# Performance work log

Hardware: AMD Instinct MI355X
Metric: run time of the kernel (lower is better)

## Reference

```python
import jax, jax.numpy as jnp
import numpy as np

EMB = 1024
FFN = 4096
H = 16
HD = EMB // H
EPS = 1e-6
SLOPE = 0.01


def leaky_relu(x):
    return jnp.where(x >= 0, x, SLOPE * x)


def layer_norm(x, g, b):
    mu = jnp.mean(x, axis=-1, keepdims=True)
    var = jnp.mean((x - mu) ** 2, axis=-1, keepdims=True)
    return (x - mu) * jax.lax.rsqrt(var + EPS) * g + b


def setup_inputs() -> dict:
    key = jax.random.key(0)
    ks = jax.random.split(key, 16)
    B, N = 2, 2048
    x = jax.random.normal(ks[0], (B, N, EMB), dtype=jnp.float32)

    def lin(k, fan_in, fan_out, kaiming_normal):
        kw, kb = jax.random.split(k)
        gain = float(np.sqrt(2.0 / (1.0 + SLOPE ** 2)))
        if kaiming_normal:
            W = jax.random.normal(kw, (fan_out, fan_in)) * (gain / np.sqrt(fan_in))
        else:
            bound = gain * np.sqrt(3.0 / fan_in)
            W = jax.random.uniform(kw, (fan_out, fan_in), minval=-bound, maxval=bound)
        b = jax.random.normal(kb, (fan_out,)) * 1e-6
        return W.astype(jnp.float32), b.astype(jnp.float32)

    Wq, bq = lin(ks[1], EMB, EMB, True)
    Wk, bk = lin(ks[2], EMB, EMB, True)
    Wv, bv = lin(ks[3], EMB, EMB, True)
    Wo, bo = lin(ks[4], EMB, EMB, True)
    W1, b1 = lin(ks[5], EMB, FFN, False)
    W2, b2 = lin(ks[6], FFN, EMB, False)
    return {
        "x": x,
        "ln1_g": jnp.ones((EMB,)), "ln1_b": jnp.zeros((EMB,)),
        "ln2_g": jnp.ones((EMB,)), "ln2_b": jnp.zeros((EMB,)),
        "Wq": Wq, "bq": bq, "Wk": Wk, "bk": bk, "Wv": Wv, "bv": bv,
        "Wo": Wo, "bo": bo, "W1": W1, "b1": b1, "W2": W2, "b2": b2,
    }


def reference(x, ln1_g, ln1_b, ln2_g, ln2_b, Wq, bq, Wk, bk, Wv, bv, Wo, bo, W1, b1, W2, b2):
    B, N, _ = x.shape
    h = x
    xn = layer_norm(x, ln1_g, ln1_b)
    # QKV projections, split heads: [B, H, N, HD]
    def heads(t):
        return t.reshape(B, N, H, HD).transpose(0, 2, 1, 3)
    q = heads(xn @ Wq.T + bq)
    k = heads(xn @ Wk.T + bk)
    v = heads(xn @ Wv.T + bv)
    scores = jnp.einsum('bhnd,bhmd->bhnm', q, k) / jnp.sqrt(jnp.float32(HD))
    probs = leaky_relu(scores)  # non-softmax attention
    ctx = jnp.einsum('bhnm,bhmd->bhnd', probs, v)
    ctx = ctx.transpose(0, 2, 1, 3).reshape(B, N, EMB)
    attn_out = ctx @ Wo.T + bo
    x = attn_out + h
    h = x
    xn = layer_norm(x, ln2_g, ln2_b)
    ff = leaky_relu(xn @ W1.T + b1) @ W2.T + b2
    return ff + h
```

## Files before the change

### kernel.cpp

```cpp
#include <hip/hip_runtime.h>
#include <hip/hip_bf16.h>


typedef unsigned short u16;
typedef __bf16 bf16x8 __attribute__((ext_vector_type(8)));
typedef float f32x4 __attribute__((ext_vector_type(4)));
typedef unsigned short u16x8 __attribute__((ext_vector_type(8)));

typedef const __attribute__((address_space(1))) void* as1cv;
typedef __attribute__((address_space(3))) void* as3v;

#define MFMA16(a, b, c) __builtin_amdgcn_mfma_f32_16x16x32_bf16((a), (b), (c), 0, 0, 0)
#define GLL16(g, l) __builtin_amdgcn_global_load_lds((as1cv)(g), (as3v)(l), 16, 0, 0)

__device__ __forceinline__ u16 f2bf(float f) {
  unsigned u = __builtin_bit_cast(unsigned, f);
  u += 0x7fffu + ((u >> 16) & 1u);
  return (u16)(u >> 16);
}
__device__ __forceinline__ float bf2f(u16 u) {
  return __builtin_bit_cast(float, ((unsigned)u) << 16);
}
__device__ __forceinline__ float lrelu(float v) { return v >= 0.f ? v : 0.01f * v; }

__device__ __forceinline__ int xcds(int bid, int nwg) {
  int cpx = nwg >> 3;
  return (bid & 7) * cpx + (bid >> 3);
}

__global__ __launch_bounds__(256) void cvt6(
    const float* __restrict__ p0, const float* __restrict__ p1,
    const float* __restrict__ p2, const float* __restrict__ p3,
    const float* __restrict__ p4, const float* __restrict__ p5,
    u16* __restrict__ o0, u16* __restrict__ o1, u16* __restrict__ o2,
    u16* __restrict__ o3, u16* __restrict__ o4, u16* __restrict__ o5)
{
  int i = blockIdx.x * 256 + threadIdx.x;
  const float* src; u16* dst; int off;
  if (i < 4 * 131072) {
    int s = i >> 17; off = i & 131071;
    src = (s == 0) ? p0 : (s == 1) ? p1 : (s == 2) ? p2 : p3;
    dst = (s == 0) ? o0 : (s == 1) ? o1 : (s == 2) ? o2 : o3;
  } else {
    int j = i - 4 * 131072;
    int s = j >> 19; off = j & 524287;
    src = s ? p5 : p4;
    dst = s ? o5 : o4;
  }
  const float4* s4 = (const float4*)src;
  float4 a = s4[(size_t)off * 2], b = s4[(size_t)off * 2 + 1];
  u16x8 o = { f2bf(a.x), f2bf(a.y), f2bf(a.z), f2bf(a.w),
              f2bf(b.x), f2bf(b.y), f2bf(b.z), f2bf(b.w) };
  *(u16x8*)(dst + (size_t)off * 8) = o;
}

__global__ __launch_bounds__(256) void ln_k(
    const float* __restrict__ x, const float* __restrict__ g,
    const float* __restrict__ bb, u16* __restrict__ out)
{
  const int tid = threadIdx.x;
  const int row = blockIdx.x;
  const float4* xr = (const float4*)(x + (size_t)row * 1024);
  float4 v = xr[tid];
  float s  = v.x + v.y + v.z + v.w;
  float s2 = v.x*v.x + v.y*v.y + v.z*v.z + v.w*v.w;
#pragma unroll
  for (int o = 32; o > 0; o >>= 1) { s += __shfl_down(s, o, 64); s2 += __shfl_down(s2, o, 64); }
  __shared__ float sh[8];
  if ((tid & 63) == 0) { sh[tid >> 6] = s; sh[4 + (tid >> 6)] = s2; }
  __syncthreads();
  s  = sh[0] + sh[1] + sh[2] + sh[3];
  s2 = sh[4] + sh[5] + sh[6] + sh[7];
  float mu  = s * (1.0f / 1024.0f);
  float var = s2 * (1.0f / 1024.0f) - mu * mu;
  float rs  = rsqrtf(var + 1e-6f);
  float4 gv = ((const float4*)g)[tid];
  float4 bv = ((const float4*)bb)[tid];
  ushort4 o;
  o.x = f2bf((v.x - mu) * rs * gv.x + bv.x);
  o.y = f2bf((v.y - mu) * rs * gv.y + bv.y);
  o.z = f2bf((v.z - mu) * rs * gv.z + bv.z);
  o.w = f2bf((v.w - mu) * rs * gv.w + bv.w);
  ((ushort4*)out)[(size_t)row * 256 + tid] = o;
}

__device__ __forceinline__ void gemm_core128(
    const u16* __restrict__ A, const u16* __restrict__ W,
    int kstride, int klen,
    int row0, int wrow0, u16* lsA, u16* lsB, f32x4 (&acc)[4][4])
{
  const int tid  = threadIdx.x;
  const int lane = tid & 63, wave = tid >> 6;
  const int wr = wave >> 1, wc = wave & 1;
  const int lr = lane & 15, lg = lane >> 4;

  const u16* ga0 = A + (size_t)(row0 + (tid >> 2)) * kstride + (tid & 3) * 8;
  const u16* ga1 = ga0 + (size_t)64 * kstride;
  const u16* gb0 = W + (size_t)(wrow0 + (tid >> 2)) * kstride + (tid & 3) * 8;
  const u16* gb1 = gb0 + (size_t)64 * kstride;
  u16* la = lsA + tid * 8;
  u16* lb = lsB + tid * 8;

  GLL16(ga0, la); GLL16(ga1, la + 2048);
  GLL16(gb0, lb); GLL16(gb1, lb + 2048);
  ga0 += 32; ga1 += 32; gb0 += 32; gb1 += 32;
  __syncthreads();

  const int nsteps = klen >> 5;
  int cur = 0;
  for (int t = 0; t < nsteps; t++) {
    int nxt = cur ^ 1;
    if (t + 1 < nsteps) {
      GLL16(ga0, la + nxt * 4096);
      GLL16(ga1, la + nxt * 4096 + 2048);
      GLL16(gb0, lb + nxt * 4096);
      GLL16(gb1, lb + nxt * 4096 + 2048);
      ga0 += 32; ga1 += 32; gb0 += 32; gb1 += 32;
    }
    const u16* cA = lsA + cur * 4096;
    const u16* cB = lsB + cur * 4096;
    bf16x8 av[4], bv[4];
#pragma unroll
    for (int mi = 0; mi < 4; mi++)
      av[mi] = *reinterpret_cast<const bf16x8*>(cA + (wr * 64 + mi * 16 + lr) * 32 + lg * 8);
#pragma unroll
    for (int ni = 0; ni < 4; ni++)
      bv[ni] = *reinterpret_cast<const bf16x8*>(cB + (wc * 64 + ni * 16 + lr) * 32 + lg * 8);
#pragma unroll
    for (int mi = 0; mi < 4; mi++)
#pragma unroll
      for (int ni = 0; ni < 4; ni++)
        acc[mi][ni] = MFMA16(av[mi], bv[ni], acc[mi][ni]);
    __syncthreads();
    cur = nxt;
  }
}

__global__ __launch_bounds__(256, 4) void gemm_qkv(
    const u16* __restrict__ xn,
    const u16* __restrict__ Wq, const u16* __restrict__ Wk, const u16* __restrict__ Wv,
    const float* __restrict__ bq, const float* __restrict__ bk, const float* __restrict__ bv,
    u16* __restrict__ qb, u16* __restrict__ kb, u16* __restrict__ vtb)
{
  __shared__ u16 lsA[2 * 128 * 32];
  __shared__ u16 lsB[2 * 128 * 32];
  const int wid = xcds(blockIdx.x, 768);
  const int mt = wid / 24, nt = wid % 24;
  const int row0 = mt * 128, col0 = nt * 128;
  const int sel = col0 >> 10, c0 = col0 & 1023;
  const u16* W = (sel == 0) ? Wq : (sel == 1) ? Wk : Wv;
  const float* bias = (sel == 0) ? bq : (sel == 1) ? bk : bv;

  f32x4 acc[4][4];
  f32x4 z = {0.f, 0.f, 0.f, 0.f};
#pragma unroll
  for (int mi = 0; mi < 4; mi++)
#pragma unroll
    for (int ni = 0; ni < 4; ni++) acc[mi][ni] = z;

  gemm_core128(xn, W, 1024, 1024, row0, c0, lsA, lsB, acc);

  const int lane = threadIdx.x & 63, wave = threadIdx.x >> 6;
  const int wr = wave >> 1, wc = wave & 1;
  const int lr = lane & 15, lg = lane >> 4;
#pragma unroll
  for (int ni = 0; ni < 4; ni++) {
    int c = c0 + wc * 64 + ni * 16 + lr;
    float bsv = bias[c];
    int h = c >> 6, hd = c & 63;
#pragma unroll
    for (int mi = 0; mi < 4; mi++) {
      int rbase = row0 + wr * 64 + mi * 16 + lg * 4;
      int b = rbase >> 11;
      int n = rbase & 2047;
      if (sel < 2) {
        u16* dst = (sel == 0) ? qb : kb;
        size_t base = ((size_t)(b * 16 + h) * 2048 + n) * 64 + hd;
#pragma unroll
        for (int r = 0; r < 4; r++)
          dst[base + (size_t)r * 64] = f2bf(acc[mi][ni][r] + bsv);
      } else {
        size_t base = ((size_t)((b * 16 + h) * 64 + hd)) * 2048 + n;
        ushort4 o;
        o.x = f2bf(acc[mi][ni][0] + bsv);
        o.y = f2bf(acc[mi][ni][1] + bsv);
        o.z = f2bf(acc[mi][ni][2] + bsv);
        o.w = f2bf(acc[mi][ni][3] + bsv);
        *(ushort4*)(vtb + base) = o;
      }
    }
  }
}

template <int EPI>
__global__ __launch_bounds__(256, 4) void gemm128(
    const u16* __restrict__ A, const u16* __restrict__ W,
    const float* __restrict__ bias, float* __restrict__ outf,
    u16* __restrict__ outh, const float* __restrict__ extra,
    int K, int nTiles, int nwg)
{
  __shared__ u16 lsA[2 * 128 * 32];
  __shared__ u16 lsB[2 * 128 * 32];
  const int wid = xcds(blockIdx.x, nwg);
  const int mt = wid / nTiles, nt = wid % nTiles;
  const int row0 = mt * 128, col0 = nt * 128;

  f32x4 acc[4][4];
  f32x4 z = {0.f, 0.f, 0.f, 0.f};
#pragma unroll
  for (int mi = 0; mi < 4; mi++)
#pragma unroll
    for (int ni = 0; ni < 4; ni++) acc[mi][ni] = z;

  gemm_core128(A, W, K, K, row0, col0, lsA, lsB, acc);

  const int N = nTiles * 128;
  const int lane = threadIdx.x & 63, wave = threadIdx.x >> 6;
  const int wr = wave >> 1, wc = wave & 1;
  const int lr = lane & 15, lg = lane >> 4;
#pragma unroll
  for (int ni = 0; ni < 4; ni++) {
    int col = col0 + wc * 64 + ni * 16 + lr;
    float bsv = bias[col];
#pragma unroll
    for (int mi = 0; mi < 4; mi++) {
      int rbase = row0 + wr * 64 + mi * 16 + lg * 4;
#pragma unroll
      for (int r = 0; r < 4; r++) {
        float v = acc[mi][ni][r] + bsv;
        size_t idx = (size_t)(rbase + r) * N + col;
        if (EPI == 0) {
          outf[idx] = v + extra[idx];
        } else {
          outh[idx] = f2bf(lrelu(v));
        }
      }
    }
  }
}

__global__ __launch_bounds__(256, 4) void gemm_ffn2(
    const u16* __restrict__ A, const u16* __restrict__ W,
    u16* __restrict__ pout)
{
  __shared__ u16 lsA[2 * 128 * 32];
  __shared__ u16 lsB[2 * 128 * 32];
  const int wid = xcds(blockIdx.x, 1024);
  const int chunk = wid >> 8, rem = wid & 255;
  const int mt = rem >> 3, nt = rem & 7;
  const int row0 = mt * 128, col0 = nt * 128;

  f32x4 acc[4][4];
  f32x4 z = {0.f, 0.f, 0.f, 0.f};
#pragma unroll
  for (int mi = 0; mi < 4; mi++)
#pragma unroll
    for (int ni = 0; ni < 4; ni++) acc[mi][ni] = z;

  gemm_core128(A + chunk * 1024, W + chunk * 1024, 4096, 1024,
               row0, col0, lsA, lsB, acc);

  u16* out = pout + (size_t)chunk * (4096 * 1024);
  const int lane = threadIdx.x & 63, wave = threadIdx.x >> 6;
  const int wr = wave >> 1, wc = wave & 1;
  const int lr = lane & 15, lg = lane >> 4;
#pragma unroll
  for (int ni = 0; ni < 4; ni++) {
    int col = col0 + wc * 64 + ni * 16 + lr;
#pragma unroll
    for (int mi = 0; mi < 4; mi++) {
      int rbase = row0 + wr * 64 + mi * 16 + lg * 4;
#pragma unroll
      for (int r = 0; r < 4; r++)
        out[(size_t)(rbase + r) * 1024 + col] = f2bf(acc[mi][ni][r]);
    }
  }
}

__global__ __launch_bounds__(256) void reduce_ffn2(
    const u16* __restrict__ p, const float* __restrict__ b2,
    const float* __restrict__ x2, float* __restrict__ out)
{
  size_t i = ((size_t)blockIdx.x * 256 + threadIdx.x) * 4;
  int col = (int)(i & 1023);
  ushort4 a0 = *(const ushort4*)(p + i);
  ushort4 a1 = *(const ushort4*)(p + (size_t)(4096 * 1024) + i);
  ushort4 a2 = *(const ushort4*)(p + (size_t)(2 * 4096 * 1024) + i);
  ushort4 a3 = *(const ushort4*)(p + (size_t)(3 * 4096 * 1024) + i);
  float4 bv = *(const float4*)(b2 + col);
  float4 xv = *(const float4*)(x2 + i);
  float4 r;
  r.x = bf2f(a0.x) + bf2f(a1.x) + bf2f(a2.x) + bf2f(a3.x) + bv.x + xv.x;
  r.y = bf2f(a0.y) + bf2f(a1.y) + bf2f(a2.y) + bf2f(a3.y) + bv.y + xv.y;
  r.z = bf2f(a0.z) + bf2f(a1.z) + bf2f(a2.z) + bf2f(a3.z) + bv.z + xv.z;
  r.w = bf2f(a0.w) + bf2f(a1.w) + bf2f(a2.w) + bf2f(a3.w) + bv.w + xv.w;
  *(float4*)(out + i) = r;
}

__device__ __forceinline__ int swz(int row, int col) {
  return row * 64 + (col ^ ((row & 7) << 3));
}

__global__ __launch_bounds__(256, 3) void attn_k(
    const u16* __restrict__ qb, const u16* __restrict__ kb,
    const u16* __restrict__ vtb, u16* __restrict__ ctx)
{
  __shared__ u16 lq[128 * 64];
  __shared__ u16 lk[64 * 64];
  __shared__ u16 lv[64 * 64];
  __shared__ u16 lp[128 * 64];

  const int tid = threadIdx.x;
  const int lane = tid & 63, wave = tid >> 6;
  const int wr = wave >> 1, wc = wave & 1;
  const int lr = lane & 15, lg = lane >> 4;
  const int wid = xcds(blockIdx.x, 512);
  const int bh = wid >> 4, qt = wid & 15;
  const int n0 = qt * 128;
  const u16* qh = qb + (size_t)bh * 2048 * 64;
  const u16* kh = kb + (size_t)bh * 2048 * 64;
  const u16* vh = vtb + (size_t)bh * 64 * 2048;

  {
    int r = tid >> 3, kk = (tid & 7) * 8;
#pragma unroll
    for (int j = 0; j < 4; j++)
      *(u16x8*)(lq + swz(j * 32 + r, kk)) =
          *(const u16x8*)(qh + (size_t)(n0 + j * 32 + r) * 64 + kk);
  }

  f32x4 z = {0.f, 0.f, 0.f, 0.f};
  f32x4 cacc[4][2];
#pragma unroll
  for (int mi = 0; mi < 4; mi++)
#pragma unroll
    for (int ni = 0; ni < 2; ni++) cacc[mi][ni] = z;

  for (int kt = 0; kt < 32; kt++) {
    {
      int r = tid >> 3, kk = (tid & 7) * 8;
#pragma unroll
      for (int j = 0; j < 2; j++) {
        *(u16x8*)(lk + swz(j * 32 + r, kk)) =
            *(const u16x8*)(kh + (size_t)(kt * 64 + j * 32 + r) * 64 + kk);
        *(u16x8*)(lv + swz(j * 32 + r, kk)) =
            *(const u16x8*)(vh + (size_t)(j * 32 + r) * 2048 + kt * 64 + kk);
      }
    }
    __syncthreads();

    f32x4 sacc[4][2];
#pragma unroll
    for (int mi = 0; mi < 4; mi++)
#pragma unroll
      for (int ni = 0; ni < 2; ni++) sacc[mi][ni] = z;
#pragma unroll
    for (int ks = 0; ks < 2; ks++) {
      bf16x8 aq[4], bk8[2];
#pragma unroll
      for (int mi = 0; mi < 4; mi++)
        aq[mi] = *reinterpret_cast<const bf16x8*>(lq + swz(wr * 64 + mi * 16 + lr, ks * 32 + lg * 8));
#pragma unroll
      for (int ni = 0; ni < 2; ni++)
        bk8[ni] = *reinterpret_cast<const bf16x8*>(lk + swz(wc * 32 + ni * 16 + lr, ks * 32 + lg * 8));
#pragma unroll
      for (int mi = 0; mi < 4; mi++)
#pragma unroll
        for (int ni = 0; ni < 2; ni++)
          sacc[mi][ni] = MFMA16(aq[mi], bk8[ni], sacc[mi][ni]);
    }
#pragma unroll
    for (int mi = 0; mi < 4; mi++)
#pragma unroll
      for (int ni = 0; ni < 2; ni++)
#pragma unroll
        for (int r = 0; r < 4; r++) {
          float v = lrelu(sacc[mi][ni][r] * 0.125f);
          int i = wr * 64 + mi * 16 + lg * 4 + r;
          int j = wc * 32 + ni * 16 + lr;
          lp[swz(i, j)] = f2bf(v);
        }
    __syncthreads();

#pragma unroll
    for (int js = 0; js < 2; js++) {
      bf16x8 pa[4], vb[2];
#pragma unroll
      for (int mi = 0; mi < 4; mi++)
        pa[mi] = *reinterpret_cast<const bf16x8*>(lp + swz(wr * 64 + mi * 16 + lr, js * 32 + lg * 8));
#pragma unroll
      for (int ni = 0; ni < 2; ni++)
        vb[ni] = *reinterpret_cast<const bf16x8*>(lv + swz(wc * 32 + ni * 16 + lr, js * 32 + lg * 8));
#pragma unroll
      for (int mi = 0; mi < 4; mi++)
#pragma unroll
        for (int ni = 0; ni < 2; ni++)
          cacc[mi][ni] = MFMA16(pa[mi], vb[ni], cacc[mi][ni]);
    }
    __syncthreads();
  }

  const int b = bh >> 4, h = bh & 15;
#pragma unroll
  for (int mi = 0; mi < 4; mi++)
#pragma unroll
    for (int ni = 0; ni < 2; ni++)
#pragma unroll
      for (int r = 0; r < 4; r++) {
        int n = n0 + wr * 64 + mi * 16 + lg * 4 + r;
        int d = wc * 32 + ni * 16 + lr;
        ctx[((size_t)(b * 2048 + n)) * 1024 + h * 64 + d] = f2bf(cacc[mi][ni][r]);
      }
}

extern "C" void kernel_launch(void* const* d_in, const int* in_sizes, int n_in,
                              void* d_out, int out_size, void* d_ws, size_t ws_size,
                              hipStream_t stream) {
  (void)in_sizes; (void)n_in; (void)out_size; (void)ws_size;
  const float* x    = (const float*)d_in[0];
  const float* ln1g = (const float*)d_in[1];
  const float* ln1b = (const float*)d_in[2];
  const float* ln2g = (const float*)d_in[3];
  const float* ln2b = (const float*)d_in[4];
  const float* Wq = (const float*)d_in[5];  const float* bq = (const float*)d_in[6];
  const float* Wk = (const float*)d_in[7];  const float* bk = (const float*)d_in[8];
  const float* Wv = (const float*)d_in[9];  const float* bv = (const float*)d_in[10];
  const float* Wo = (const float*)d_in[11]; const float* bo = (const float*)d_in[12];
  const float* W1 = (const float*)d_in[13]; const float* b1 = (const float*)d_in[14];
  const float* W2 = (const float*)d_in[15]; const float* b2 = (const float*)d_in[16];

  char* ws = (char*)d_ws;
  u16*   WqB  = (u16*)(ws + ((size_t)0 << 20));
  u16*   WkB  = (u16*)(ws + ((size_t)2 << 20));
  u16*   WvB  = (u16*)(ws + ((size_t)4 << 20));
  u16*   WoB  = (u16*)(ws + ((size_t)6 << 20));
  u16*   W1B  = (u16*)(ws + ((size_t)8 << 20));
  u16*   W2B  = (u16*)(ws + ((size_t)16 << 20));
  u16*   xn1  = (u16*)(ws + ((size_t)24 << 20));
  u16*   qb   = (u16*)(ws + ((size_t)32 << 20));
  u16*   kb   = (u16*)(ws + ((size_t)40 << 20));
  u16*   vtb  = (u16*)(ws + ((size_t)48 << 20));
  u16*   ctxb = (u16*)(ws + ((size_t)56 << 20));
  float* x2   = (float*)(ws + ((size_t)64 << 20));
  u16*   xn2  = (u16*)(ws + ((size_t)80 << 20));
  u16*   ff1  = (u16*)(ws + ((size_t)88 << 20));
  u16*   pF2  = (u16*)(ws + ((size_t)24 << 20));

  dim3 blk(256);

  cvt6<<<dim3(6144), blk, 0, stream>>>(Wq, Wk, Wv, Wo, W1, W2,
                                       WqB, WkB, WvB, WoB, W1B, W2B);
  ln_k<<<dim3(4096), blk, 0, stream>>>(x, ln1g, ln1b, xn1);
  gemm_qkv<<<dim3(768), blk, 0, stream>>>(xn1, WqB, WkB, WvB, bq, bk, bv,
                                          qb, kb, vtb);
  attn_k<<<dim3(512), blk, 0, stream>>>(qb, kb, vtb, ctxb);
  gemm128<0><<<dim3(256), blk, 0, stream>>>(ctxb, WoB, bo, x2, (u16*)nullptr, x,
                                            1024, 8, 256);
  ln_k<<<dim3(4096), blk, 0, stream>>>(x2, ln2g, ln2b, xn2);
  gemm128<1><<<dim3(1024), blk, 0, stream>>>(xn2, W1B, b1, (float*)nullptr, ff1,
                                             (const float*)nullptr, 1024, 32, 1024);
  gemm_ffn2<<<dim3(1024), blk, 0, stream>>>(ff1, W2B, pF2);
  reduce_ffn2<<<dim3(4096), blk, 0, stream>>>(pF2, b2, x2, (float*)d_out);
}
```

Measured before the change: 353.4 us.

## Rewrite attention kernel with register-resident Q, transposed scores, and async KV pipeline

The attention kernel now keeps each wave's Q rows in registers and computes transposed score tiles (K·Q). Their MFMA output layout feeds straight into a 16x16x16 MFMA against V^T as the B operand, so the LDS round-trip for the probability matrix goes away. K/V tiles are streamed with global_load_lds into a 4-deep ring buffer with manual vmcnt waits and a single barrier per tile, replacing three __syncthreads per tile. The 1/sqrt(d) scale is folded into the Q projection epilogue and leaky ReLU becomes fmax. The cost is more LDS per block, occupancy lowered to 2 blocks, and more MFMA instructions from the smaller-K variant.

```diff
diff --git a/kernel.cpp b/kernel.cpp
--- a/kernel.cpp
+++ b/kernel.cpp
@@ -3,9 +3,13 @@
 
 
 typedef unsigned short u16;
+typedef unsigned int u32;
 typedef __bf16 bf16x8 __attribute__((ext_vector_type(8)));
+typedef __bf16 bf16x4 __attribute__((ext_vector_type(4)));
 typedef float f32x4 __attribute__((ext_vector_type(4)));
 typedef unsigned short u16x8 __attribute__((ext_vector_type(8)));
+typedef unsigned int u32x2 __attribute__((ext_vector_type(2)));
+typedef short s16x4 __attribute__((ext_vector_type(4)));
 
 typedef const __attribute__((address_space(1))) void* as1cv;
 typedef __attribute__((address_space(3))) void* as3v;
@@ -21,7 +25,19 @@
 __device__ __forceinline__ float bf2f(u16 u) {
   return __builtin_bit_cast(float, ((unsigned)u) << 16);
 }
-__device__ __forceinline__ float lrelu(float v) { return v >= 0.f ? v : 0.01f * v; }
+__device__ __forceinline__ float lrelu(float v) { return fmaxf(v, 0.01f * v); }
+
+__device__ __forceinline__ void mfma16x16(f32x4& c, bf16x4 a, bf16x4 b) {
+#if __has_builtin(__builtin_amdgcn_mfma_f32_16x16x16bf16_1k)
+  c = __builtin_amdgcn_mfma_f32_16x16x16bf16_1k(
+      __builtin_bit_cast(s16x4, a), __builtin_bit_cast(s16x4, b), c, 0, 0, 0);
+#else
+  u32x2 au = __builtin_bit_cast(u32x2, a);
+  u32x2 bu = __builtin_bit_cast(u32x2, b);
+  asm volatile("s_nop 2\n\tv_mfma_f32_16x16x16_bf16 %0, %1, %2, %0"
+               : "+v"(c) : "v"(au), "v"(bu));
+#endif
+}
 
 __device__ __forceinline__ int xcds(int bid, int nwg) {
   int cpx = nwg >> 3;
@@ -163,6 +179,7 @@
   const int lane = threadIdx.x & 63, wave = threadIdx.x >> 6;
   const int wr = wave >> 1, wc = wave & 1;
   const int lr = lane & 15, lg = lane >> 4;
+  const float qscale = (sel == 0) ? 0.125f : 1.0f;
 #pragma unroll
   for (int ni = 0; ni < 4; ni++) {
     int c = c0 + wc * 64 + ni * 16 + lr;
@@ -178,7 +195,7 @@
         size_t base = ((size_t)(b * 16 + h) * 2048 + n) * 64 + hd;
 #pragma unroll
         for (int r = 0; r < 4; r++)
-          dst[base + (size_t)r * 64] = f2bf(acc[mi][ni][r] + bsv);
+          dst[base + (size_t)r * 64] = f2bf((acc[mi][ni][r] + bsv) * qscale);
       } else {
         size_t base = ((size_t)((b * 16 + h) * 64 + hd)) * 2048 + n;
         ushort4 o;
@@ -297,22 +314,14 @@
   *(float4*)(out + i) = r;
 }
 
-__device__ __forceinline__ int swz(int row, int col) {
-  return row * 64 + (col ^ ((row & 7) << 3));
-}
-
-__global__ __launch_bounds__(256, 3) void attn_k(
+__global__ __launch_bounds__(256, 2) void attn_k(
     const u16* __restrict__ qb, const u16* __restrict__ kb,
     const u16* __restrict__ vtb, u16* __restrict__ ctx)
 {
-  __shared__ u16 lq[128 * 64];
-  __shared__ u16 lk[64 * 64];
-  __shared__ u16 lv[64 * 64];
-  __shared__ u16 lp[128 * 64];
+  __shared__ u16 lds[4 * 8192];
 
   const int tid = threadIdx.x;
-  const int lane = tid & 63, wave = tid >> 6;
-  const int wr = wave >> 1, wc = wave & 1;
+  const int lane = tid & 63, wq = tid >> 6;
   const int lr = lane & 15, lg = lane >> 4;
   const int wid = xcds(blockIdx.x, 512);
   const int bh = wid >> 4, qt = wid & 15;
@@ -321,96 +330,99 @@
   const u16* kh = kb + (size_t)bh * 2048 * 64;
   const u16* vh = vtb + (size_t)bh * 64 * 2048;
 
-  {
-    int r = tid >> 3, kk = (tid & 7) * 8;
-#pragma unroll
-    for (int j = 0; j < 4; j++)
-      *(u16x8*)(lq + swz(j * 32 + r, kk)) =
-          *(const u16x8*)(qh + (size_t)(n0 + j * 32 + r) * 64 + kk);
-  }
+  const int srow = tid >> 3;
+  const int sgg  = (tid & 7) ^ (srow & 7);
+  const size_t koff0 = (size_t)srow * 64 + sgg * 8;
+  const size_t koff1 = koff0 + (size_t)32 * 64;
+  const size_t voff0 = (size_t)srow * 2048 + sgg * 8;
+  const size_t voff1 = voff0 + (size_t)32 * 2048;
+  const int dk0 = tid * 8, dk1 = tid * 8 + 2048;
+
+#define STAGE_KV(t, jb)                                              \
+  {                                                                  \
+    const u16* ks_ = kh + (size_t)(t) * 4096;                        \
+    const u16* vs_ = vh + (t) * 64;                                  \
+    u16* lb_ = lds + (jb) * 8192;                                    \
+    GLL16(ks_ + koff0, lb_ + dk0);                                   \
+    GLL16(ks_ + koff1, lb_ + dk1);                                   \
+    GLL16(vs_ + voff0, lb_ + 4096 + dk0);                            \
+    GLL16(vs_ + voff1, lb_ + 4096 + dk1);                            \
+  }
+
+  STAGE_KV(0, 0);
+  STAGE_KV(1, 1);
+
+  bf16x8 qr[2][2];
+#pragma unroll
+  for (int qi = 0; qi < 2; qi++)
+#pragma unroll
+    for (int ks = 0; ks < 2; ks++)
+      qr[qi][ks] = *(const bf16x8*)(
+          qh + (size_t)(n0 + wq * 32 + qi * 16 + lr) * 64 + ks * 32 + lg * 8);
+  asm volatile("" ::: "memory");
 
   f32x4 z = {0.f, 0.f, 0.f, 0.f};
   f32x4 cacc[4][2];
 #pragma unroll
-  for (int mi = 0; mi < 4; mi++)
-#pragma unroll
-    for (int ni = 0; ni < 2; ni++) cacc[mi][ni] = z;
-
-  for (int kt = 0; kt < 32; kt++) {
-    {
-      int r = tid >> 3, kk = (tid & 7) * 8;
-#pragma unroll
-      for (int j = 0; j < 2; j++) {
-        *(u16x8*)(lk + swz(j * 32 + r, kk)) =
-            *(const u16x8*)(kh + (size_t)(kt * 64 + j * 32 + r) * 64 + kk);
-        *(u16x8*)(lv + swz(j * 32 + r, kk)) =
-            *(const u16x8*)(vh + (size_t)(j * 32 + r) * 2048 + kt * 64 + kk);
+  for (int di = 0; di < 4; di++) { cacc[di][0] = z; cacc[di][1] = z; }
+
+  const int lswz = lr & 7;
+  for (int kt4 = 0; kt4 < 8; kt4++) {
+#pragma unroll
+    for (int j = 0; j < 4; j++) {
+      const int t = kt4 * 4 + j;
+      if (j == 3 && kt4 == 7) asm volatile("s_waitcnt vmcnt(0)" ::: "memory");
+      else                    asm volatile("s_waitcnt vmcnt(4)" ::: "memory");
+      __builtin_amdgcn_s_barrier();
+      asm volatile("" ::: "memory");
+      if (kt4 < 7 || j < 2) STAGE_KV(t + 2, (j + 2) & 3);
+
+      const u16* lk = lds + j * 8192;
+      const u16* lv = lds + j * 8192 + 4096;
+#pragma unroll
+      for (int ki = 0; ki < 4; ki++) {
+        f32x4 s0 = z, s1 = z;
+#pragma unroll
+        for (int ks = 0; ks < 2; ks++) {
+          bf16x8 kf = *(const bf16x8*)(
+              lk + (ki * 16 + lr) * 64 + (((ks * 4 + lg) ^ lswz) * 8));
+          s0 = MFMA16(kf, qr[0][ks], s0);
+          s1 = MFMA16(kf, qr[1][ks], s1);
+        }
+        bf16x4 p0, p1;
+#pragma unroll
+        for (int r = 0; r < 4; r++) {
+          p0[r] = (__bf16)lrelu(s0[r]);
+          p1[r] = (__bf16)lrelu(s1[r]);
+        }
+#pragma unroll
+        for (int di = 0; di < 4; di++) {
+          bf16x4 vf = *(const bf16x4*)(
+              lv + (di * 16 + lr) * 64 +
+              (((ki * 2 + (lg >> 1)) ^ lswz) * 8) + (lg & 1) * 4);
+          mfma16x16(cacc[di][0], vf, p0);
+          mfma16x16(cacc[di][1], vf, p1);
+        }
       }
     }
-    __syncthreads();
-
-    f32x4 sacc[4][2];
-#pragma unroll
-    for (int mi = 0; mi < 4; mi++)
-#pragma unroll
-      for (int ni = 0; ni < 2; ni++) sacc[mi][ni] = z;
-#pragma unroll
-    for (int ks = 0; ks < 2; ks++) {
-      bf16x8 aq[4], bk8[2];
-#pragma unroll
-      for (int mi = 0; mi < 4; mi++)
-        aq[mi] = *reinterpret_cast<const bf16x8*>(lq + swz(wr * 64 + mi * 16 + lr, ks * 32 + lg * 8));
-#pragma unroll
-      for (int ni = 0; ni < 2; ni++)
-        bk8[ni] = *reinterpret_cast<const bf16x8*>(lk + swz(wc * 32 + ni * 16 + lr, ks * 32 + lg * 8));
-#pragma unroll
-      for (int mi = 0; mi < 4; mi++)
-#pragma unroll
-        for (int ni = 0; ni < 2; ni++)
-          sacc[mi][ni] = MFMA16(aq[mi], bk8[ni], sacc[mi][ni]);
-    }
-#pragma unroll
-    for (int mi = 0; mi < 4; mi++)
-#pragma unroll
-      for (int ni = 0; ni < 2; ni++)
-#pragma unroll
-        for (int r = 0; r < 4; r++) {
-          float v = lrelu(sacc[mi][ni][r] * 0.125f);
-          int i = wr * 64 + mi * 16 + lg * 4 + r;
-          int j = wc * 32 + ni * 16 + lr;
-          lp[swz(i, j)] = f2bf(v);
-        }
-    __syncthreads();
-
-#pragma unroll
-    for (int js = 0; js < 2; js++) {
-      bf16x8 pa[4], vb[2];
-#pragma unroll
-      for (int mi = 0; mi < 4; mi++)
-        pa[mi] = *reinterpret_cast<const bf16x8*>(lp + swz(wr * 64 + mi * 16 + lr, js * 32 + lg * 8));
-#pragma unroll
-      for (int ni = 0; ni < 2; ni++)
-        vb[ni] = *reinterpret_cast<const bf16x8*>(lv + swz(wc * 32 + ni * 16 + lr, js * 32 + lg * 8));
-#pragma unroll
-      for (int mi = 0; mi < 4; mi++)
-#pragma unroll
-        for (int ni = 0; ni < 2; ni++)
-          cacc[mi][ni] = MFMA16(pa[mi], vb[ni], cacc[mi][ni]);
-    }
-    __syncthreads();
   }
 
   const int b = bh >> 4, h = bh & 15;
 #pragma unroll
-  for (int mi = 0; mi < 4; mi++)
-#pragma unroll
-    for (int ni = 0; ni < 2; ni++)
-#pragma unroll
-      for (int r = 0; r < 4; r++) {
-        int n = n0 + wr * 64 + mi * 16 + lg * 4 + r;
-        int d = wc * 32 + ni * 16 + lr;
-        ctx[((size_t)(b * 2048 + n)) * 1024 + h * 64 + d] = f2bf(cacc[mi][ni][r]);
-      }
+  for (int qi = 0; qi < 2; qi++) {
+    int n = n0 + wq * 32 + qi * 16 + lr;
+    u16* op = ctx + ((size_t)(b * 2048 + n)) * 1024 + h * 64;
+#pragma unroll
+    for (int di = 0; di < 4; di++) {
+      ushort4 o;
+      o.x = f2bf(cacc[di][qi][0]);
+      o.y = f2bf(cacc[di][qi][1]);
+      o.z = f2bf(cacc[di][qi][2]);
+      o.w = f2bf(cacc[di][qi][3]);
+      *(ushort4*)(op + di * 16 + lg * 4) = o;
+    }
+  }
+#undef STAGE_KV
 }
 
 extern "C" void kernel_launch(void* const* d_in, const int* in_sizes, int n_in,
```

Result: no change. 353.4 us (+0.0%).
